# Kernel tuning notes

Measured on AMD Instinct MI355X. Metric: run time of the kernel, lower is better.

The kernel has to match this reference:

```python
import jax, jax.numpy as jnp
import numpy as np
import math

HIDDEN = 1024
NUM_HEADS = 16
HEAD_DIM = 64
NUM_PREV = 4
BATCH = 4
SEQ = 1024
ROPE_BASE = 10000.0


def _rope(x):
    """Apply rotary embedding to x [..., seq, head_dim] (rotate-half form)."""
    d = x.shape[-1]
    s = x.shape[-2]
    inv_freq = 1.0 / (ROPE_BASE ** (jnp.arange(0, d, 2, dtype=jnp.float32) / d))
    ang = jnp.arange(s, dtype=jnp.float32)[:, None] * inv_freq[None, :]  # [s, d/2]
    cos, sin = jnp.cos(ang), jnp.sin(ang)
    x1, x2 = jnp.split(x, 2, axis=-1)
    return jnp.concatenate([x1 * cos - x2 * sin, x1 * sin + x2 * cos], axis=-1)


def setup_inputs() -> dict:
    key = jax.random.key(0)
    ks = jax.random.split(key, 8)
    std = 0.02
    d = {
        "hidden_states": jax.random.normal(ks[0], (BATCH, SEQ, HIDDEN), jnp.float32),
        "prev_hidden_states": jax.random.normal(ks[1], (NUM_PREV, BATCH, SEQ, HIDDEN), jnp.float32),
        "wq": jax.random.normal(ks[2], (HIDDEN, NUM_HEADS * HEAD_DIM), jnp.float32) * std,
        "bq": jnp.zeros((NUM_HEADS * HEAD_DIM,), jnp.float32),
        "wk": jax.random.normal(ks[3], (HIDDEN, NUM_HEADS * HEAD_DIM), jnp.float32) * std,
        "bk": jnp.zeros((NUM_HEADS * HEAD_DIM,), jnp.float32),
        "wv": jax.random.normal(ks[4], (HIDDEN, NUM_HEADS * HEAD_DIM), jnp.float32) * std,
        "bv": jnp.zeros((NUM_HEADS * HEAD_DIM,), jnp.float32),
        "wo": jax.random.normal(ks[5], (NUM_HEADS * HEAD_DIM, HIDDEN), jnp.float32) * std,
        "bo": jnp.zeros((HIDDEN,), jnp.float32),
        "wg": jax.random.normal(ks[6], (HIDDEN, NUM_PREV), jnp.float32) * std,
    }
    return d


def reference(hidden_states, prev_hidden_states, wq, bq, wk, bk, wv, bv, wo, bo, wg):
    B, S, H = hidden_states.shape
    P = prev_hidden_states.shape[0]
    nh, hd = NUM_HEADS, HEAD_DIM

    # Q projection + split heads + RoPE: [b, h, s, d]
    q = (hidden_states @ wq + bq).reshape(B, S, nh, hd).transpose(0, 2, 1, 3)
    q = _rope(q)

    # K/V projections for all prev layers at once: [p, b, h, s, d]
    k = (jnp.einsum('pbsh,he->pbse', prev_hidden_states, wk) + bk)
    k = k.reshape(P, B, S, nh, hd).transpose(0, 1, 3, 2, 4)
    k = _rope(k)
    v = (jnp.einsum('pbsh,he->pbse', prev_hidden_states, wv) + bv)
    v = v.reshape(P, B, S, nh, hd).transpose(0, 1, 3, 2, 4)

    # Attention per prev layer
    scale = 1.0 / math.sqrt(hd)
    attn = jnp.einsum('bhqd,pbhkd->pbhqk', q, k) * scale
    attn = jax.nn.softmax(attn, axis=-1)
    out = jnp.einsum('pbhqk,pbhkd->pbhqd', attn, v)  # [p, b, h, s, d]
    out = out.transpose(0, 1, 3, 2, 4).reshape(P, B, S, H)

    # Learned layer gating (faithful to original broadcast: requires B == P)
    pooled = jnp.mean(hidden_states, axis=1)            # [b, hidden]
    layer_w = jax.nn.softmax(pooled @ wg, axis=-1)      # [b, p]
    combined = jnp.sum(out * layer_w[:, :, None, None], axis=0)  # [b, s, hidden]

    return combined @ wo + bo
```

## Files before the change

### kernel.cpp

```cpp
#include <hip/hip_runtime.h>
#include <hip/hip_bf16.h>

#define B_  4
#define S_  1024
#define H_  1024
#define NH  16
#define HD  64
#define P_  4

typedef __attribute__((ext_vector_type(8))) short bf16x8;
typedef __attribute__((ext_vector_type(4))) float f32x4;
typedef __attribute__((ext_vector_type(16))) float f32x16;
typedef __attribute__((ext_vector_type(4))) unsigned int u32x4;

__device__ __forceinline__ float b2f(short s) {
  union { unsigned int u; float f; } v;
  v.u = ((unsigned int)(unsigned short)s) << 16;
  return v.f;
}
__device__ __forceinline__ short f2b(float f) {
  __hip_bfloat16 h = __float2bfloat16(f);
  return *reinterpret_cast<short*>(&h);
}
__device__ __forceinline__ float fast_exp2(float x) {
  float r;
  asm volatile("v_exp_f32 %0, %1" : "=v"(r) : "v"(x));
  return r;
}
__device__ __forceinline__ void gload_lds16(const void* g, void* l) {
  __builtin_amdgcn_global_load_lds(
      (const __attribute__((address_space(1))) unsigned int*)((uintptr_t)g),
      (__attribute__((address_space(3))) unsigned int*)((uintptr_t)l),
      16, 0, 0);
}

__global__ void prep_kernel(const float* __restrict__ hidden, const float* __restrict__ prev,
                            const float* __restrict__ wq, const float* __restrict__ wk,
                            const float* __restrict__ wv, const float* __restrict__ wo,
                            short* __restrict__ hbf, short* __restrict__ pbf,
                            short* __restrict__ wqT, short* __restrict__ wkT,
                            short* __restrict__ wvT, short* __restrict__ woT,
                            float* __restrict__ cost, float* __restrict__ sint,
                            float* __restrict__ pooled) {
  __shared__ short tile[32][33];
  int bid = blockIdx.x, tid = threadIdx.x;
  if (bid < 10240) {
    const float* src; short* dst; int idx;
    if (bid < 2048) { src = hidden; dst = hbf; idx = bid * 256 + tid; }
    else            { src = prev;   dst = pbf; idx = (bid - 2048) * 256 + tid; }
    const float4* s4 = (const float4*)(src + (size_t)idx * 8);
    float4 a = s4[0], b = s4[1];
    bf16x8 pk;
    pk[0] = f2b(a.x); pk[1] = f2b(a.y); pk[2] = f2b(a.z); pk[3] = f2b(a.w);
    pk[4] = f2b(b.x); pk[5] = f2b(b.y); pk[6] = f2b(b.z); pk[7] = f2b(b.w);
    *(bf16x8*)(dst + (size_t)idx * 8) = pk;
  } else if (bid < 14336) {
    int tb = bid - 10240;
    int z = tb >> 10, t = tb & 1023;
    const float* src = (z == 0) ? wq : (z == 1) ? wk : (z == 2) ? wv : wo;
    short*       dst = (z == 0) ? wqT : (z == 1) ? wkT : (z == 2) ? wvT : woT;
    int tx = tid & 31, ty = tid >> 5;
    int c0 = (t & 31) * 32, r0 = (t >> 5) * 32;
#pragma unroll
    for (int i = 0; i < 4; ++i)
      tile[ty + 8 * i][tx] = f2b(src[(r0 + ty + 8 * i) * 1024 + c0 + tx]);
    __syncthreads();
#pragma unroll
    for (int i = 0; i < 4; ++i)
      dst[(c0 + ty + 8 * i) * 1024 + r0 + tx] = tile[tx][ty + 8 * i];
  } else if (bid < 14464) {
    int idx = (bid - 14336) * 256 + tid;
    int s = idx >> 5, i = idx & 31;
    float invf = expf(-(float)i * (logf(10000.0f) / 32.0f));
    float a = (float)s * invf;
    cost[idx] = cosf(a);
    sint[idx] = sinf(a);
  } else {
    int idx = (bid - 14464) * 256 + tid;
    int b = idx >> 10, e = idx & 1023;
    const float* hp = hidden + (size_t)b * S_ * H_ + e;
    float s = 0.f;
    for (int t = 0; t < S_; ++t) s += hp[t * H_];
    pooled[idx] = s * (1.0f / 1024.0f);
  }
}

__global__ void gate_kernel(const float* __restrict__ pooled, const float* __restrict__ wg,
                            float* __restrict__ lw) {
  int w = threadIdx.x >> 6, lane = threadIdx.x & 63;
  float a0 = 0.f, a1 = 0.f, a2 = 0.f, a3 = 0.f;
  for (int e = lane; e < 1024; e += 64) {
    float pv = pooled[w * 1024 + e];
    a0 += pv * wg[e * 4 + 0];
    a1 += pv * wg[e * 4 + 1];
    a2 += pv * wg[e * 4 + 2];
    a3 += pv * wg[e * 4 + 3];
  }
#pragma unroll
  for (int off = 32; off > 0; off >>= 1) {
    a0 += __shfl_xor(a0, off, 64);
    a1 += __shfl_xor(a1, off, 64);
    a2 += __shfl_xor(a2, off, 64);
    a3 += __shfl_xor(a3, off, 64);
  }
  if (lane == 0) {
    float mx = fmaxf(fmaxf(a0, a1), fmaxf(a2, a3));
    float e0 = expf(a0 - mx), e1 = expf(a1 - mx), e2 = expf(a2 - mx), e3 = expf(a3 - mx);
    float inv = 1.0f / (e0 + e1 + e2 + e3);
    lw[w * 4 + 0] = e0 * inv;
    lw[w * 4 + 1] = e1 * inv;
    lw[w * 4 + 2] = e2 * inv;
    lw[w * 4 + 3] = e3 * inv;
  }
}

__device__ __forceinline__ void rope_epilogue(const f32x4 (&acc)[4][4], const float* __restrict__ bias,
                                              short* __restrict__ outp,
                                              const float* __restrict__ cost,
                                              const float* __restrict__ sint,
                                              int m0, int wm, int quad, int c, int hh) {
  float b0 = bias[hh * 64 + c];
  float b1 = bias[hh * 64 + 16 + c];
  float b2_ = bias[hh * 64 + 32 + c];
  float b3 = bias[hh * 64 + 48 + c];
#pragma unroll
  for (int mt = 0; mt < 4; ++mt) {
    int gm = m0 + wm * 64 + mt * 16 + quad * 4;
#pragma unroll
    for (int j = 0; j < 4; ++j) {
      int m = gm + j;
      int s = m & 1023;
      int bbx = m >> 10;
      int orow = ((bbx * NH + hh) * S_ + s) * HD;
      float c0f = cost[s * 32 + c], s0f = sint[s * 32 + c];
      float x1 = acc[mt][0][j] + b0, x2 = acc[mt][2][j] + b2_;
      outp[orow + c]      = f2b(x1 * c0f - x2 * s0f);
      outp[orow + 32 + c] = f2b(x1 * s0f + x2 * c0f);
      float c1f = cost[s * 32 + 16 + c], s1f = sint[s * 32 + 16 + c];
      float y1 = acc[mt][1][j] + b1, y2 = acc[mt][3][j] + b3;
      outp[orow + 16 + c] = f2b(y1 * c1f - y2 * s1f);
      outp[orow + 48 + c] = f2b(y1 * s1f + y2 * c1f);
    }
  }
}

__launch_bounds__(256, 2)
__global__ void qkv_gemm(const short* __restrict__ hbf, const short* __restrict__ pbf,
                         const short* __restrict__ BTq, const short* __restrict__ BTk,
                         const short* __restrict__ BTv,
                         const float* __restrict__ bq, const float* __restrict__ bk,
                         const float* __restrict__ bv,
                         short* __restrict__ outq, short* __restrict__ outk,
                         short* __restrict__ outv,
                         const float* __restrict__ cost, const float* __restrict__ sint) {
  __shared__ __align__(16) short As[128 * 64];
  __shared__ __align__(16) short Bs1[128 * 64];
  __shared__ __align__(16) short Bs2[128 * 64];
  int id = blockIdx.x;
  int xcd = id & 7;
  int local = id >> 3;
  int n0i = local & 7;
  int yl = local >> 3;
  int y = yl * 8 + xcd;
  int tid = threadIdx.x;
  int lane = tid & 63, wvv = tid >> 6;
  int quad = lane >> 4, c = lane & 15;
  int wm = wvv & 1, wn = wvv >> 1;
  bool isQ = y < 32;
  int m0 = (isQ ? y : (y - 32)) * 128;
  int n0 = n0i * 128;
  const short* A  = isQ ? hbf : pbf;
  const short* B1 = isQ ? BTq : BTk;
  f32x4 acc1[4][4] = {}, acc2[4][4] = {};
  const short* Ab = A + (size_t)m0 * 1024;
  const short* Bb1 = B1 + (size_t)n0 * 1024;
  const short* Bb2 = BTv + (size_t)n0 * 1024;
  int sr = tid >> 3, sch = tid & 7;

  for (int kb = 0; kb < 16; ++kb) {
    int k0 = kb * 64;
    __syncthreads();
#pragma unroll
    for (int rd = 0; rd < 4; ++rd) {
      int row = sr + rd * 32;
      int col = ((sch ^ (row & 7)) * 8) + k0;
      gload_lds16(Ab + row * 1024 + col,  As  + rd * 2048 + tid * 8);
      gload_lds16(Bb1 + row * 1024 + col, Bs1 + rd * 2048 + tid * 8);
      if (!isQ) gload_lds16(Bb2 + row * 1024 + col, Bs2 + rd * 2048 + tid * 8);
    }
    __syncthreads();
#pragma unroll
    for (int ko = 0; ko < 2; ++ko) {
      bf16x8 af[4], b1f[4];
#pragma unroll
      for (int mt = 0; mt < 4; ++mt) {
        int row = wm * 64 + mt * 16 + c;
        af[mt] = *(const bf16x8*)&As[row * 64 + (((ko * 4 + quad) ^ (row & 7)) * 8)];
      }
#pragma unroll
      for (int nt = 0; nt < 4; ++nt) {
        int row = wn * 64 + nt * 16 + c;
        b1f[nt] = *(const bf16x8*)&Bs1[row * 64 + (((ko * 4 + quad) ^ (row & 7)) * 8)];
      }
#pragma unroll
      for (int mt = 0; mt < 4; ++mt)
#pragma unroll
        for (int nt = 0; nt < 4; ++nt)
          acc1[mt][nt] = __builtin_amdgcn_mfma_f32_16x16x32_bf16(af[mt], b1f[nt], acc1[mt][nt], 0, 0, 0);
      if (!isQ) {
        bf16x8 b2f_[4];
#pragma unroll
        for (int nt = 0; nt < 4; ++nt) {
          int row = wn * 64 + nt * 16 + c;
          b2f_[nt] = *(const bf16x8*)&Bs2[row * 64 + (((ko * 4 + quad) ^ (row & 7)) * 8)];
        }
#pragma unroll
        for (int mt = 0; mt < 4; ++mt)
#pragma unroll
          for (int nt = 0; nt < 4; ++nt)
            acc2[mt][nt] = __builtin_amdgcn_mfma_f32_16x16x32_bf16(af[mt], b2f_[nt], acc2[mt][nt], 0, 0, 0);
      }
    }
  }

  int colb = n0 + wn * 64;
  int hh = colb >> 6;
  if (isQ) {
    rope_epilogue(acc1, bq, outq, cost, sint, m0, wm, quad, c, hh);
  } else {
    rope_epilogue(acc1, bk, outk, cost, sint, m0, wm, quad, c, hh);
    float bb[4];
#pragma unroll
    for (int nt = 0; nt < 4; ++nt) bb[nt] = bv[hh * 64 + nt * 16 + c];
#pragma unroll
    for (int mt = 0; mt < 4; ++mt) {
      int gm = m0 + wm * 64 + mt * 16 + quad * 4;
      int s4 = gm & 1023, pb = gm >> 10;
#pragma unroll
      for (int nt = 0; nt < 4; ++nt) {
        int d = nt * 16 + c;
        ushort4 pk;
        pk.x = (unsigned short)f2b(acc2[mt][nt][0] + bb[nt]);
        pk.y = (unsigned short)f2b(acc2[mt][nt][1] + bb[nt]);
        pk.z = (unsigned short)f2b(acc2[mt][nt][2] + bb[nt]);
        pk.w = (unsigned short)f2b(acc2[mt][nt][3] + bb[nt]);
        *(ushort4*)&outv[((pb * NH + hh) * HD + d) * S_ + s4] = pk;
      }
    }
  }
}

__launch_bounds__(256, 4)
__global__ void attn_kernel(const short* __restrict__ q, const short* __restrict__ k,
                            const short* __restrict__ vt, short* __restrict__ o) {
  int blk = blockIdx.x;
  int x = blk & 7, qt = (blk >> 3) & 7, g = blk >> 6;
  int pbh = g * 8 + x;
  int b = (pbh >> 4) & 3, h = pbh & 15;
  int tid = threadIdx.x;
  int w = tid >> 6, lane = tid & 63;
  int l31 = lane & 31, hh = lane >> 5;
  int r7 = l31 & 7;

  __shared__ __align__(16) short Klds[64 * 64];
  __shared__ __align__(16) short Vlds[64 * 64];
  __shared__ float lsumf[4][32];

  const short* qbase = q + ((size_t)(b * NH + h) * S_ + qt * 128 + w * 32 + l31) * HD + hh * 8;
  bf16x8 aq[4];
#pragma unroll
  for (int st4 = 0; st4 < 4; ++st4) aq[st4] = *(const bf16x8*)(qbase + st4 * 16);

  const short* kb = k + (size_t)pbh * S_ * HD;
  const short* vb = vt + (size_t)pbh * HD * S_;

  f32x16 O0 = {}, O1 = {};
  float ls0 = 0.f, ls1 = 0.f, ls2 = 0.f, ls3 = 0.f;
  const float cs = 0.18033688011f;

  int sr = tid >> 3;
  int lc = (tid & 7) ^ (sr & 7);

  for (int kt = 0; kt < 16; ++kt) {
    __syncthreads();
    const short* ksrc = kb + (kt * 64 + sr) * HD + lc * 8;
    gload_lds16(ksrc,           Klds + tid * 8);
    gload_lds16(ksrc + 32 * HD, Klds + 2048 + tid * 8);
    const short* vsrc = vb + (size_t)sr * S_ + kt * 64 + lc * 8;
    gload_lds16(vsrc,           Vlds + tid * 8);
    gload_lds16(vsrc + 32 * S_, Vlds + 2048 + tid * 8);
    __syncthreads();

    u32x4 pa[4];
#pragma unroll
    for (int tau = 0; tau < 2; ++tau) {
      f32x16 st = {};
#pragma unroll
      for (int step = 0; step < 4; ++step) {
        bf16x8 kf = *(const bf16x8*)&Klds[(tau * 32 + l31) * 64 + (((step * 2 + hh) ^ r7) * 8)];
        st = __builtin_amdgcn_mfma_f32_32x32x16_bf16(kf, aq[step], st, 0, 0, 0);
      }
      unsigned wb[8];
#pragma unroll
      for (int m = 0; m < 8; ++m) {
        float p0 = fast_exp2(st[2 * m] * cs);
        float p1 = fast_exp2(st[2 * m + 1] * cs);
        float ps = p0 + p1;
        if ((m & 3) == 0) ls0 += ps;
        else if ((m & 3) == 1) ls1 += ps;
        else if ((m & 3) == 2) ls2 += ps;
        else ls3 += ps;
        asm("v_cvt_pk_bf16_f32 %0, %1, %2" : "=v"(wb[m]) : "v"(p0), "v"(p1));
      }
#pragma unroll
      for (int gg = 0; gg < 2; ++gg) {
        unsigned x0 = wb[4 * gg + 0], y0 = wb[4 * gg + 2];
        unsigned x1 = wb[4 * gg + 1], y1 = wb[4 * gg + 3];
        asm volatile("v_permlane32_swap_b32 %0, %1" : "+v"(x0), "+v"(y0));
        asm volatile("v_permlane32_swap_b32 %0, %1" : "+v"(x1), "+v"(y1));
        u32x4 paw;
        paw[0] = x0; paw[1] = x1; paw[2] = y0; paw[3] = y1;
        pa[2 * tau + gg] = paw;
      }
    }

#pragma unroll
    for (int T = 0; T < 4; ++T) {
      bf16x8 ap = __builtin_bit_cast(bf16x8, pa[T]);
      bf16x8 vf0 = *(const bf16x8*)&Vlds[l31 * 64 + (((T * 2 + hh) ^ r7) * 8)];
      O0 = __builtin_amdgcn_mfma_f32_32x32x16_bf16(ap, vf0, O0, 0, 0, 0);
      bf16x8 vf1 = *(const bf16x8*)&Vlds[(32 + l31) * 64 + (((T * 2 + hh) ^ r7) * 8)];
      O1 = __builtin_amdgcn_mfma_f32_32x32x16_bf16(ap, vf1, O1, 0, 0, 0);
    }
  }

  float lsum = (ls0 + ls1) + (ls2 + ls3);
  lsum += __shfl_xor(lsum, 32, 64);
  if (lane < 32) lsumf[w][l31] = lsum;

  short* ob = o + ((size_t)pbh * S_ + qt * 128 + w * 32) * HD;
#pragma unroll
  for (int gg = 0; gg < 4; ++gg) {
    f32x4 lv = *(const f32x4*)&lsumf[w][4 * hh + 8 * gg];
#pragma unroll
    for (int j = 0; j < 4; ++j) {
      float inv = 1.0f / lv[j];
      int qrow = 4 * hh + 8 * gg + j;
      ob[qrow * HD + l31]      = f2b(O0[4 * gg + j] * inv);
      ob[qrow * HD + 32 + l31] = f2b(O1[4 * gg + j] * inv);
    }
  }
}

__global__ void combine_kernel(const short* __restrict__ o, const float* __restrict__ lw,
                               short* __restrict__ comb) {
  int idx = blockIdx.x * 256 + threadIdx.x;
  int e8 = idx & 127;
  int s = (idx >> 7) & 1023;
  int b = idx >> 17;
  int h = e8 >> 3, d0 = (e8 & 7) * 8;
  float acc[8] = {};
#pragma unroll
  for (int p = 0; p < 4; ++p) {
    float wgt = lw[p * 4 + b];
    const short* op = o + (((size_t)(p * 4 + b) * NH + h) * S_ + s) * HD + d0;
    bf16x8 v = *(const bf16x8*)op;
#pragma unroll
    for (int i = 0; i < 8; ++i) acc[i] += wgt * b2f(v[i]);
  }
  bf16x8 pk;
#pragma unroll
  for (int i = 0; i < 8; ++i) pk[i] = f2b(acc[i]);
  *(bf16x8*)&comb[((size_t)b * S_ + s) * H_ + e8 * 8] = pk;
}

__launch_bounds__(256, 4)
__global__ void gemm_out(const short* __restrict__ A, const short* __restrict__ BT,
                         const float* __restrict__ bias, float* __restrict__ outf) {
  __shared__ __align__(16) short As[64 * 64];
  __shared__ __align__(16) short Bs[128 * 64];
  int id = blockIdx.x;
  int xcd = id & 7;
  int local = id >> 3;
  int n0i = local & 7;
  int yl = local >> 3;
  int y = yl * 8 + xcd;
  int tid = threadIdx.x;
  int lane = tid & 63, wvv = tid >> 6;
  int quad = lane >> 4, c = lane & 15;
  int wm = wvv & 1, wn = wvv >> 1;
  int m0 = y * 64, n0 = n0i * 128;
  f32x4 acc[2][4] = {};
  const short* Ab = A + (size_t)m0 * 1024;
  const short* Bb = BT + (size_t)n0 * 1024;
  int sr = tid >> 3, sch = tid & 7;

  for (int kb = 0; kb < 16; ++kb) {
    int k0 = kb * 64;
    __syncthreads();
#pragma unroll
    for (int rd = 0; rd < 2; ++rd) {
      int row = sr + rd * 32;
      int col = ((sch ^ (row & 7)) * 8) + k0;
      gload_lds16(Ab + row * 1024 + col, As + rd * 2048 + tid * 8);
    }
#pragma unroll
    for (int rd = 0; rd < 4; ++rd) {
      int row = sr + rd * 32;
      int col = ((sch ^ (row & 7)) * 8) + k0;
      gload_lds16(Bb + row * 1024 + col, Bs + rd * 2048 + tid * 8);
    }
    __syncthreads();
#pragma unroll
    for (int ko = 0; ko < 2; ++ko) {
      bf16x8 af[2], bfr[4];
#pragma unroll
      for (int mt = 0; mt < 2; ++mt) {
        int row = wm * 32 + mt * 16 + c;
        af[mt] = *(const bf16x8*)&As[row * 64 + (((ko * 4 + quad) ^ (row & 7)) * 8)];
      }
#pragma unroll
      for (int nt = 0; nt < 4; ++nt) {
        int row = wn * 64 + nt * 16 + c;
        bfr[nt] = *(const bf16x8*)&Bs[row * 64 + (((ko * 4 + quad) ^ (row & 7)) * 8)];
      }
#pragma unroll
      for (int mt = 0; mt < 2; ++mt)
#pragma unroll
        for (int nt = 0; nt < 4; ++nt)
          acc[mt][nt] = __builtin_amdgcn_mfma_f32_16x16x32_bf16(af[mt], bfr[nt], acc[mt][nt], 0, 0, 0);
    }
  }

  int colb = n0 + wn * 64;
  float bb[4];
#pragma unroll
  for (int nt = 0; nt < 4; ++nt) bb[nt] = bias[colb + nt * 16 + c];
#pragma unroll
  for (int mt = 0; mt < 2; ++mt) {
    int gm = m0 + wm * 32 + mt * 16 + quad * 4;
#pragma unroll
    for (int j = 0; j < 4; ++j) {
      int m = gm + j;
#pragma unroll
      for (int nt = 0; nt < 4; ++nt)
        outf[(size_t)m * 1024 + colb + nt * 16 + c] = acc[mt][nt][j] + bb[nt];
    }
  }
}

extern "C" void kernel_launch(void* const* d_in, const int* in_sizes, int n_in,
                              void* d_out, int out_size, void* d_ws, size_t ws_size,
                              hipStream_t stream) {
  (void)in_sizes; (void)n_in; (void)out_size; (void)ws_size;
  const float* hidden = (const float*)d_in[0];
  const float* prev   = (const float*)d_in[1];
  const float* wq = (const float*)d_in[2];
  const float* bq = (const float*)d_in[3];
  const float* wk = (const float*)d_in[4];
  const float* bk = (const float*)d_in[5];
  const float* wv = (const float*)d_in[6];
  const float* bv = (const float*)d_in[7];
  const float* wo = (const float*)d_in[8];
  const float* bo = (const float*)d_in[9];
  const float* wg = (const float*)d_in[10];
  float* out = (float*)d_out;
  char* ws = (char*)d_ws;

  size_t off = 0;
  short* wqT = (short*)(ws + off); off += (size_t)1024 * 1024 * 2;
  short* wkT = (short*)(ws + off); off += (size_t)1024 * 1024 * 2;
  short* wvT = (short*)(ws + off); off += (size_t)1024 * 1024 * 2;
  short* woT = (short*)(ws + off); off += (size_t)1024 * 1024 * 2;
  short* hbf = (short*)(ws + off); off += (size_t)B_ * S_ * H_ * 2;
  short* pbf = (short*)(ws + off); off += (size_t)P_ * B_ * S_ * H_ * 2;
  short* qbf = (short*)(ws + off); off += (size_t)B_ * S_ * H_ * 2;
  short* kbf = (short*)(ws + off); off += (size_t)P_ * B_ * S_ * H_ * 2;
  short* vtb = (short*)(ws + off); off += (size_t)P_ * B_ * S_ * H_ * 2;
  float* cost = (float*)(ws + off); off += (size_t)S_ * 32 * 4;
  float* sint = (float*)(ws + off); off += (size_t)S_ * 32 * 4;
  float* pooled = (float*)(ws + off); off += (size_t)B_ * H_ * 4;
  float* lw = (float*)(ws + off); off += 64;
  short* obf  = pbf;
  short* comb = qbf;

  prep_kernel<<<14480, 256, 0, stream>>>(hidden, prev, wq, wk, wv, wo,
                                         hbf, pbf, wqT, wkT, wvT, woT,
                                         cost, sint, pooled);
  gate_kernel<<<1, 256, 0, stream>>>(pooled, wg, lw);
  qkv_gemm<<<1280, 256, 0, stream>>>(hbf, pbf, wqT, wkT, wvT,
                                     bq, bk, bv, qbf, kbf, vtb, cost, sint);
  attn_kernel<<<2048, 256, 0, stream>>>(qbf, kbf, vtb, obf);
  combine_kernel<<<2048, 256, 0, stream>>>(obf, lw, comb);
  gemm_out<<<512, 256, 0, stream>>>(comb, woT, bo, out);
}
```

Before: 381.9 us.

## Rewrite QKV GEMM as 256x256-tile, 512-thread double-buffered pipeline

The fused QKV projection GEMM is restructured. It moves from 128x128 tiles of 256 threads, where K and V shared one A tile, to 256x256 tiles of 512 threads, with Q, K and V as separate workgroups. A and B are split into half tiles and double-buffered in LDS, and loads for the next k-step are interleaved with MFMA phases using partial vmcnt waits and s_setprio. This aims to hide global-to-LDS latency and raise arithmetic intensity per tile. In exchange, K and V no longer share A loads, and per-thread register pressure is much higher.

```diff
diff --git a/kernel.cpp b/kernel.cpp
--- a/kernel.cpp
+++ b/kernel.cpp
@@ -114,37 +114,7 @@
   }
 }
 
-__device__ __forceinline__ void rope_epilogue(const f32x4 (&acc)[4][4], const float* __restrict__ bias,
-                                              short* __restrict__ outp,
-                                              const float* __restrict__ cost,
-                                              const float* __restrict__ sint,
-                                              int m0, int wm, int quad, int c, int hh) {
-  float b0 = bias[hh * 64 + c];
-  float b1 = bias[hh * 64 + 16 + c];
-  float b2_ = bias[hh * 64 + 32 + c];
-  float b3 = bias[hh * 64 + 48 + c];
-#pragma unroll
-  for (int mt = 0; mt < 4; ++mt) {
-    int gm = m0 + wm * 64 + mt * 16 + quad * 4;
-#pragma unroll
-    for (int j = 0; j < 4; ++j) {
-      int m = gm + j;
-      int s = m & 1023;
-      int bbx = m >> 10;
-      int orow = ((bbx * NH + hh) * S_ + s) * HD;
-      float c0f = cost[s * 32 + c], s0f = sint[s * 32 + c];
-      float x1 = acc[mt][0][j] + b0, x2 = acc[mt][2][j] + b2_;
-      outp[orow + c]      = f2b(x1 * c0f - x2 * s0f);
-      outp[orow + 32 + c] = f2b(x1 * s0f + x2 * c0f);
-      float c1f = cost[s * 32 + 16 + c], s1f = sint[s * 32 + 16 + c];
-      float y1 = acc[mt][1][j] + b1, y2 = acc[mt][3][j] + b3;
-      outp[orow + 16 + c] = f2b(y1 * c1f - y2 * s1f);
-      outp[orow + 48 + c] = f2b(y1 * s1f + y2 * c1f);
-    }
-  }
-}
-
-__launch_bounds__(256, 2)
+__launch_bounds__(512, 2)
 __global__ void qkv_gemm(const short* __restrict__ hbf, const short* __restrict__ pbf,
                          const short* __restrict__ BTq, const short* __restrict__ BTk,
                          const short* __restrict__ BTv,
@@ -153,98 +123,194 @@
                          short* __restrict__ outq, short* __restrict__ outk,
                          short* __restrict__ outv,
                          const float* __restrict__ cost, const float* __restrict__ sint) {
-  __shared__ __align__(16) short As[128 * 64];
-  __shared__ __align__(16) short Bs1[128 * 64];
-  __shared__ __align__(16) short Bs2[128 * 64];
+  __shared__ __align__(16) short As[2][2][8192];
+  __shared__ __align__(16) short Bs[2][2][8192];
+
   int id = blockIdx.x;
-  int xcd = id & 7;
-  int local = id >> 3;
-  int n0i = local & 7;
-  int yl = local >> 3;
-  int y = yl * 8 + xcd;
+  int wg = (id & 7) * 72 + (id >> 3);
+  int matrix, mt_, nt_;
+  if (wg < 64)       { matrix = 0; int l = wg;       mt_ = l >> 2; nt_ = l & 3; }
+  else if (wg < 320) { matrix = 1; int l = wg - 64;  mt_ = l >> 2; nt_ = l & 3; }
+  else               { matrix = 2; int l = wg - 320; mt_ = l >> 2; nt_ = l & 3; }
+  int m0 = mt_ * 256, n0 = nt_ * 256;
+  const short* A  = (matrix == 0) ? hbf : pbf;
+  const short* BT = (matrix == 0) ? BTq : (matrix == 1) ? BTk : BTv;
+  const short* Ab = A + (size_t)m0 * 1024;
+  const short* Bb = BT + (size_t)n0 * 1024;
+
   int tid = threadIdx.x;
-  int lane = tid & 63, wvv = tid >> 6;
+  int lane = tid & 63, wv = tid >> 6;
   int quad = lane >> 4, c = lane & 15;
-  int wm = wvv & 1, wn = wvv >> 1;
-  bool isQ = y < 32;
-  int m0 = (isQ ? y : (y - 32)) * 128;
-  int n0 = n0i * 128;
-  const short* A  = isQ ? hbf : pbf;
-  const short* B1 = isQ ? BTq : BTk;
-  f32x4 acc1[4][4] = {}, acc2[4][4] = {};
-  const short* Ab = A + (size_t)m0 * 1024;
-  const short* Bb1 = B1 + (size_t)n0 * 1024;
-  const short* Bb2 = BTv + (size_t)n0 * 1024;
-  int sr = tid >> 3, sch = tid & 7;
-
-  for (int kb = 0; kb < 16; ++kb) {
-    int k0 = kb * 64;
-    __syncthreads();
-#pragma unroll
-    for (int rd = 0; rd < 4; ++rd) {
-      int row = sr + rd * 32;
-      int col = ((sch ^ (row & 7)) * 8) + k0;
-      gload_lds16(Ab + row * 1024 + col,  As  + rd * 2048 + tid * 8);
-      gload_lds16(Bb1 + row * 1024 + col, Bs1 + rd * 2048 + tid * 8);
-      if (!isQ) gload_lds16(Bb2 + row * 1024 + col, Bs2 + rd * 2048 + tid * 8);
-    }
-    __syncthreads();
-#pragma unroll
-    for (int ko = 0; ko < 2; ++ko) {
-      bf16x8 af[4], b1f[4];
-#pragma unroll
-      for (int mt = 0; mt < 4; ++mt) {
-        int row = wm * 64 + mt * 16 + c;
-        af[mt] = *(const bf16x8*)&As[row * 64 + (((ko * 4 + quad) ^ (row & 7)) * 8)];
-      }
+  int wm = wv >> 2, wn = wv & 3;
+
+  f32x4 acc[8][4] = {};
+  bf16x8 afr[4][2], bfr[4][2];
+
+  int r0row = tid >> 3,        r0ch = tid & 7;
+  int r1row = (512 + tid) >> 3, r1ch = tid & 7;
+  int b0n = (r0row >> 5) * 64 + (r0row & 31);
+  int b1n = (r1row >> 5) * 64 + (r1row & 31);
+  int a0c = (r0ch ^ (r0row & 7)) * 8;
+  int a1c = (r1ch ^ (r1row & 7)) * 8;
+
+#define STAGE_A(buf, h, k0s) do {                                              \
+    gload_lds16(Ab + (size_t)((h)*128 + r0row) * 1024 + (k0s) + a0c,           \
+                &As[buf][h][tid * 8]);                                         \
+    gload_lds16(Ab + (size_t)((h)*128 + r1row) * 1024 + (k0s) + a1c,           \
+                &As[buf][h][(512 + tid) * 8]);                                 \
+  } while (0)
+#define STAGE_B(buf, h, k0s) do {                                              \
+    gload_lds16(Bb + (size_t)(b0n + (h)*32) * 1024 + (k0s) + a0c,              \
+                &Bs[buf][h][tid * 8]);                                         \
+    gload_lds16(Bb + (size_t)(b1n + (h)*32) * 1024 + (k0s) + a1c,              \
+                &Bs[buf][h][(512 + tid) * 8]);                                 \
+  } while (0)
+#define PIPE_SYNC4() do {                                                      \
+    asm volatile("s_waitcnt vmcnt(4)" ::: "memory");                           \
+    __builtin_amdgcn_s_barrier();                                              \
+    __builtin_amdgcn_sched_barrier(0);                                         \
+  } while (0)
+
+  STAGE_A(0, 0, 0);
+  STAGE_B(0, 0, 0);
+  STAGE_B(0, 1, 0);
+  STAGE_A(0, 1, 0);
+
+#pragma unroll 1
+  for (int t = 0; t < 16; ++t) {
+    int cur = t & 1, nc = cur ^ 1;
+    int k0 = t * 64;
+    int kn = (t < 15) ? k0 + 64 : k0;
+
+    PIPE_SYNC4();
+#pragma unroll
+    for (int i = 0; i < 4; ++i) {
+      int row = wm * 64 + i * 16 + c;
+      const short* base = &As[cur][0][row * 64];
+#pragma unroll
+      for (int ko = 0; ko < 2; ++ko)
+        afr[i][ko] = *(const bf16x8*)&base[(((ko * 4 + quad) ^ (row & 7)) * 8)];
+    }
+#pragma unroll
+    for (int nt = 0; nt < 2; ++nt) {
+      int bl = wn * 32 + nt * 16 + c;
+      const short* base = &Bs[cur][0][bl * 64];
+#pragma unroll
+      for (int ko = 0; ko < 2; ++ko)
+        bfr[nt][ko] = *(const bf16x8*)&base[(((ko * 4 + quad) ^ (bl & 7)) * 8)];
+    }
+    STAGE_A(nc, 0, kn);
+    __builtin_amdgcn_s_setprio(1);
+#pragma unroll
+    for (int i = 0; i < 4; ++i)
+#pragma unroll
+      for (int nt = 0; nt < 2; ++nt)
+#pragma unroll
+        for (int ko = 0; ko < 2; ++ko)
+          acc[i][nt] = __builtin_amdgcn_mfma_f32_16x16x32_bf16(afr[i][ko], bfr[nt][ko], acc[i][nt], 0, 0, 0);
+    __builtin_amdgcn_s_setprio(0);
+
+    PIPE_SYNC4();
+#pragma unroll
+    for (int nt = 2; nt < 4; ++nt) {
+      int bl = wn * 32 + (nt & 1) * 16 + c;
+      const short* base = &Bs[cur][1][bl * 64];
+#pragma unroll
+      for (int ko = 0; ko < 2; ++ko)
+        bfr[nt][ko] = *(const bf16x8*)&base[(((ko * 4 + quad) ^ (bl & 7)) * 8)];
+    }
+    STAGE_B(nc, 0, kn);
+    __builtin_amdgcn_s_setprio(1);
+#pragma unroll
+    for (int i = 0; i < 4; ++i)
+#pragma unroll
+      for (int nt = 2; nt < 4; ++nt)
+#pragma unroll
+        for (int ko = 0; ko < 2; ++ko)
+          acc[i][nt] = __builtin_amdgcn_mfma_f32_16x16x32_bf16(afr[i][ko], bfr[nt][ko], acc[i][nt], 0, 0, 0);
+    __builtin_amdgcn_s_setprio(0);
+
+    PIPE_SYNC4();
+#pragma unroll
+    for (int i = 0; i < 4; ++i) {
+      int row = wm * 64 + i * 16 + c;
+      const short* base = &As[cur][1][row * 64];
+#pragma unroll
+      for (int ko = 0; ko < 2; ++ko)
+        afr[i][ko] = *(const bf16x8*)&base[(((ko * 4 + quad) ^ (row & 7)) * 8)];
+    }
+    STAGE_B(nc, 1, kn);
+    __builtin_amdgcn_s_setprio(1);
+#pragma unroll
+    for (int i = 0; i < 4; ++i)
+#pragma unroll
+      for (int nt = 2; nt < 4; ++nt)
+#pragma unroll
+        for (int ko = 0; ko < 2; ++ko)
+          acc[4 + i][nt] = __builtin_amdgcn_mfma_f32_16x16x32_bf16(afr[i][ko], bfr[nt][ko], acc[4 + i][nt], 0, 0, 0);
+    __builtin_amdgcn_s_setprio(0);
+
+    STAGE_A(nc, 1, kn);
+    __builtin_amdgcn_s_setprio(1);
+#pragma unroll
+    for (int i = 0; i < 4; ++i)
+#pragma unroll
+      for (int nt = 0; nt < 2; ++nt)
+#pragma unroll
+        for (int ko = 0; ko < 2; ++ko)
+          acc[4 + i][nt] = __builtin_amdgcn_mfma_f32_16x16x32_bf16(afr[i][ko], bfr[nt][ko], acc[4 + i][nt], 0, 0, 0);
+    __builtin_amdgcn_s_setprio(0);
+  }
+#undef STAGE_A
+#undef STAGE_B
+#undef PIPE_SYNC4
+
+  asm volatile("s_waitcnt vmcnt(0)" ::: "memory");
+
+  int hh = (n0 >> 6) + wn;
+  if (matrix <= 1) {
+    const float* bias = (matrix == 0) ? bq : bk;
+    short* outp = (matrix == 0) ? outq : outk;
+    float b0 = bias[hh * 64 + c];
+    float b1 = bias[hh * 64 + 16 + c];
+    float b2_ = bias[hh * 64 + 32 + c];
+    float b3 = bias[hh * 64 + 48 + c];
+#pragma unroll
+    for (int mt = 0; mt < 8; ++mt) {
+      int gmb = m0 + (mt >> 2) * 128 + wm * 64 + (mt & 3) * 16 + quad * 4;
+#pragma unroll
+      for (int j = 0; j < 4; ++j) {
+        int m = gmb + j;
+        int s = m & 1023;
+        int bbx = m >> 10;
+        size_t orow = ((size_t)(bbx * NH + hh) * S_ + s) * HD;
+        float c0f = cost[s * 32 + c], s0f = sint[s * 32 + c];
+        float x1 = acc[mt][0][j] + b0, x2 = acc[mt][2][j] + b2_;
+        outp[orow + c]      = f2b(x1 * c0f - x2 * s0f);
+        outp[orow + 32 + c] = f2b(x1 * s0f + x2 * c0f);
+        float c1f = cost[s * 32 + 16 + c], s1f = sint[s * 32 + 16 + c];
+        float y1 = acc[mt][1][j] + b1, y2 = acc[mt][3][j] + b3;
+        outp[orow + 16 + c] = f2b(y1 * c1f - y2 * s1f);
+        outp[orow + 48 + c] = f2b(y1 * s1f + y2 * c1f);
+      }
+    }
+  } else {
+    float bb[4];
+#pragma unroll
+    for (int nt = 0; nt < 4; ++nt) bb[nt] = bv[hh * 64 + (nt >> 1) * 32 + (nt & 1) * 16 + c];
+#pragma unroll
+    for (int mt = 0; mt < 8; ++mt) {
+      int gmb = m0 + (mt >> 2) * 128 + wm * 64 + (mt & 3) * 16 + quad * 4;
+      int s4 = gmb & 1023, pb = gmb >> 10;
 #pragma unroll
       for (int nt = 0; nt < 4; ++nt) {
-        int row = wn * 64 + nt * 16 + c;
-        b1f[nt] = *(const bf16x8*)&Bs1[row * 64 + (((ko * 4 + quad) ^ (row & 7)) * 8)];
-      }
-#pragma unroll
-      for (int mt = 0; mt < 4; ++mt)
-#pragma unroll
-        for (int nt = 0; nt < 4; ++nt)
-          acc1[mt][nt] = __builtin_amdgcn_mfma_f32_16x16x32_bf16(af[mt], b1f[nt], acc1[mt][nt], 0, 0, 0);
-      if (!isQ) {
-        bf16x8 b2f_[4];
-#pragma unroll
-        for (int nt = 0; nt < 4; ++nt) {
-          int row = wn * 64 + nt * 16 + c;
-          b2f_[nt] = *(const bf16x8*)&Bs2[row * 64 + (((ko * 4 + quad) ^ (row & 7)) * 8)];
-        }
-#pragma unroll
-        for (int mt = 0; mt < 4; ++mt)
-#pragma unroll
-          for (int nt = 0; nt < 4; ++nt)
-            acc2[mt][nt] = __builtin_amdgcn_mfma_f32_16x16x32_bf16(af[mt], b2f_[nt], acc2[mt][nt], 0, 0, 0);
-      }
-    }
-  }
-
-  int colb = n0 + wn * 64;
-  int hh = colb >> 6;
-  if (isQ) {
-    rope_epilogue(acc1, bq, outq, cost, sint, m0, wm, quad, c, hh);
-  } else {
-    rope_epilogue(acc1, bk, outk, cost, sint, m0, wm, quad, c, hh);
-    float bb[4];
-#pragma unroll
-    for (int nt = 0; nt < 4; ++nt) bb[nt] = bv[hh * 64 + nt * 16 + c];
-#pragma unroll
-    for (int mt = 0; mt < 4; ++mt) {
-      int gm = m0 + wm * 64 + mt * 16 + quad * 4;
-      int s4 = gm & 1023, pb = gm >> 10;
-#pragma unroll
-      for (int nt = 0; nt < 4; ++nt) {
-        int d = nt * 16 + c;
+        int d = (nt >> 1) * 32 + (nt & 1) * 16 + c;
         ushort4 pk;
-        pk.x = (unsigned short)f2b(acc2[mt][nt][0] + bb[nt]);
-        pk.y = (unsigned short)f2b(acc2[mt][nt][1] + bb[nt]);
-        pk.z = (unsigned short)f2b(acc2[mt][nt][2] + bb[nt]);
-        pk.w = (unsigned short)f2b(acc2[mt][nt][3] + bb[nt]);
-        *(ushort4*)&outv[((pb * NH + hh) * HD + d) * S_ + s4] = pk;
+        pk.x = (unsigned short)f2b(acc[mt][nt][0] + bb[nt]);
+        pk.y = (unsigned short)f2b(acc[mt][nt][1] + bb[nt]);
+        pk.z = (unsigned short)f2b(acc[mt][nt][2] + bb[nt]);
+        pk.w = (unsigned short)f2b(acc[mt][nt][3] + bb[nt]);
+        *(ushort4*)&outv[(((size_t)pb * NH + hh) * HD + d) * S_ + s4] = pk;
       }
     }
   }
@@ -488,8 +554,8 @@
                                          hbf, pbf, wqT, wkT, wvT, woT,
                                          cost, sint, pooled);
   gate_kernel<<<1, 256, 0, stream>>>(pooled, wg, lw);
-  qkv_gemm<<<1280, 256, 0, stream>>>(hbf, pbf, wqT, wkT, wvT,
-                                     bq, bk, bv, qbf, kbf, vtb, cost, sint);
+  qkv_gemm<<<576, 512, 0, stream>>>(hbf, pbf, wqT, wkT, wvT,
+                                    bq, bk, bv, qbf, kbf, vtb, cost, sint);
   attn_kernel<<<2048, 256, 0, stream>>>(qbf, kbf, vtb, obf);
   combine_kernel<<<2048, 256, 0, stream>>>(obf, lw, comb);
   gemm_out<<<512, 256, 0, stream>>>(comb, woT, bo, out);
```

After: 395.9 us. +3.7%, slower.

## Double-buffer K/V tiles in attention and parallelize mean pooling across chunks

Applied to the files above, without the earlier changes.

The attention kernel now holds two LDS buffers for K and V and issues the global-to-LDS loads for the next tile before computing on the current one. A partial vmcnt wait and raw barriers replace the two __syncthreads, so the load latency can overlap with MFMA work. The mean-pooling part of the prep kernel changes from 16 long serial column sums to 128 blocks, each summing 32 rows with float4 loads into partial buffers, which the gate kernel then adds together. This doubles attention LDS use, which may lower occupancy, and relies on the vmcnt count matching the number of outstanding loads.

```diff
diff --git a/kernel.cpp b/kernel.cpp
--- a/kernel.cpp
+++ b/kernel.cpp
@@ -76,12 +76,19 @@
     cost[idx] = cosf(a);
     sint[idx] = sinf(a);
   } else {
-    int idx = (bid - 14464) * 256 + tid;
-    int b = idx >> 10, e = idx & 1023;
-    const float* hp = hidden + (size_t)b * S_ * H_ + e;
-    float s = 0.f;
-    for (int t = 0; t < S_; ++t) s += hp[t * H_];
-    pooled[idx] = s * (1.0f / 1024.0f);
+    int idx = bid - 14464;
+    int b = idx >> 5, chunk = idx & 31;
+    const float* hp = hidden + (size_t)b * S_ * H_ + (size_t)chunk * 32 * H_ + tid * 4;
+    float4 s = {0.f, 0.f, 0.f, 0.f};
+#pragma unroll 4
+    for (int t = 0; t < 32; ++t) {
+      float4 v = *(const float4*)(hp + (size_t)t * H_);
+      s.x += v.x; s.y += v.y; s.z += v.z; s.w += v.w;
+    }
+    float4 r;
+    r.x = s.x * (1.0f / 1024.0f); r.y = s.y * (1.0f / 1024.0f);
+    r.z = s.z * (1.0f / 1024.0f); r.w = s.w * (1.0f / 1024.0f);
+    *(float4*)(pooled + (size_t)(b * 32 + chunk) * 1024 + tid * 4) = r;
   }
 }
 
@@ -90,7 +97,9 @@
   int w = threadIdx.x >> 6, lane = threadIdx.x & 63;
   float a0 = 0.f, a1 = 0.f, a2 = 0.f, a3 = 0.f;
   for (int e = lane; e < 1024; e += 64) {
-    float pv = pooled[w * 1024 + e];
+    float pv = 0.f;
+#pragma unroll
+    for (int ch = 0; ch < 32; ++ch) pv += pooled[(size_t)(w * 32 + ch) * 1024 + e];
     a0 += pv * wg[e * 4 + 0];
     a1 += pv * wg[e * 4 + 1];
     a2 += pv * wg[e * 4 + 2];
@@ -262,8 +271,8 @@
   int l31 = lane & 31, hh = lane >> 5;
   int r7 = l31 & 7;
 
-  __shared__ __align__(16) short Klds[64 * 64];
-  __shared__ __align__(16) short Vlds[64 * 64];
+  __shared__ __align__(16) short Klds[2][64 * 64];
+  __shared__ __align__(16) short Vlds[2][64 * 64];
   __shared__ float lsumf[4][32];
 
   const short* qbase = q + ((size_t)(b * NH + h) * S_ + qt * 128 + w * 32 + l31) * HD + hh * 8;
@@ -281,15 +290,27 @@
   int sr = tid >> 3;
   int lc = (tid & 7) ^ (sr & 7);
 
+#define STAGE_KV(kt2, bufi) do {                                           \
+    const short* ksrc = kb + ((kt2) * 64 + sr) * HD + lc * 8;              \
+    gload_lds16(ksrc,           &Klds[bufi][tid * 8]);                     \
+    gload_lds16(ksrc + 32 * HD, &Klds[bufi][2048 + tid * 8]);              \
+    const short* vsrc = vb + (size_t)sr * S_ + (kt2) * 64 + lc * 8;        \
+    gload_lds16(vsrc,           &Vlds[bufi][tid * 8]);                     \
+    gload_lds16(vsrc + 32 * S_, &Vlds[bufi][2048 + tid * 8]);              \
+  } while (0)
+
+  STAGE_KV(0, 0);
+
   for (int kt = 0; kt < 16; ++kt) {
-    __syncthreads();
-    const short* ksrc = kb + (kt * 64 + sr) * HD + lc * 8;
-    gload_lds16(ksrc,           Klds + tid * 8);
-    gload_lds16(ksrc + 32 * HD, Klds + 2048 + tid * 8);
-    const short* vsrc = vb + (size_t)sr * S_ + kt * 64 + lc * 8;
-    gload_lds16(vsrc,           Vlds + tid * 8);
-    gload_lds16(vsrc + 32 * S_, Vlds + 2048 + tid * 8);
-    __syncthreads();
+    int cb = kt & 1;
+    if (kt < 15) {
+      STAGE_KV(kt + 1, cb ^ 1);
+      asm volatile("s_waitcnt vmcnt(4)" ::: "memory");
+    } else {
+      asm volatile("s_waitcnt vmcnt(0)" ::: "memory");
+    }
+    __builtin_amdgcn_s_barrier();
+    __builtin_amdgcn_sched_barrier(0);
 
     u32x4 pa[4];
 #pragma unroll
@@ -297,7 +318,7 @@
       f32x16 st = {};
 #pragma unroll
       for (int step = 0; step < 4; ++step) {
-        bf16x8 kf = *(const bf16x8*)&Klds[(tau * 32 + l31) * 64 + (((step * 2 + hh) ^ r7) * 8)];
+        bf16x8 kf = *(const bf16x8*)&Klds[cb][(tau * 32 + l31) * 64 + (((step * 2 + hh) ^ r7) * 8)];
         st = __builtin_amdgcn_mfma_f32_32x32x16_bf16(kf, aq[step], st, 0, 0, 0);
       }
       unsigned wb[8];
@@ -327,12 +348,15 @@
 #pragma unroll
     for (int T = 0; T < 4; ++T) {
       bf16x8 ap = __builtin_bit_cast(bf16x8, pa[T]);
-      bf16x8 vf0 = *(const bf16x8*)&Vlds[l31 * 64 + (((T * 2 + hh) ^ r7) * 8)];
+      bf16x8 vf0 = *(const bf16x8*)&Vlds[cb][l31 * 64 + (((T * 2 + hh) ^ r7) * 8)];
       O0 = __builtin_amdgcn_mfma_f32_32x32x16_bf16(ap, vf0, O0, 0, 0, 0);
-      bf16x8 vf1 = *(const bf16x8*)&Vlds[(32 + l31) * 64 + (((T * 2 + hh) ^ r7) * 8)];
+      bf16x8 vf1 = *(const bf16x8*)&Vlds[cb][(32 + l31) * 64 + (((T * 2 + hh) ^ r7) * 8)];
       O1 = __builtin_amdgcn_mfma_f32_32x32x16_bf16(ap, vf1, O1, 0, 0, 0);
     }
-  }
+
+    __builtin_amdgcn_s_barrier();
+  }
+#undef STAGE_KV
 
   float lsum = (ls0 + ls1) + (ls2 + ls3);
   lsum += __shfl_xor(lsum, 32, 64);
@@ -479,12 +503,12 @@
   short* vtb = (short*)(ws + off); off += (size_t)P_ * B_ * S_ * H_ * 2;
   float* cost = (float*)(ws + off); off += (size_t)S_ * 32 * 4;
   float* sint = (float*)(ws + off); off += (size_t)S_ * 32 * 4;
-  float* pooled = (float*)(ws + off); off += (size_t)B_ * H_ * 4;
+  float* pooled = (float*)(ws + off); off += (size_t)B_ * 32 * 1024 * 4;
   float* lw = (float*)(ws + off); off += 64;
   short* obf  = pbf;
   short* comb = qbf;
 
-  prep_kernel<<<14480, 256, 0, stream>>>(hidden, prev, wq, wk, wv, wo,
+  prep_kernel<<<14592, 256, 0, stream>>>(hidden, prev, wq, wk, wv, wo,
                                          hbf, pbf, wqT, wkT, wvT, woT,
                                          cost, sint, pooled);
   gate_kernel<<<1, 256, 0, stream>>>(pooled, wg, lw);
```

Result: faster. 348.0 us (-8.9%).
